# Performance work log

Hardware: AMD Instinct MI355X
Metric: run time of the kernel (lower is better)

The kernel has to match this reference:

```python
import jax, jax.numpy as jnp
import numpy as np

TAU = 0.5

def setup_inputs() -> dict:
    key = jax.random.key(0)
    kx, ky = jax.random.split(key)
    B, H = 8192, 256
    x = jax.random.normal(kx, (B, H), dtype=jnp.float32)
    y = jax.random.normal(ky, (B, H), dtype=jnp.float32)
    return {"x": x, "y": y}

def reference(x, y):
    # L2-normalize rows
    x_norm = x / jnp.linalg.norm(x, axis=1, keepdims=True)
    y_norm = y / jnp.linalg.norm(y, axis=1, keepdims=True)
    xy_norm = jnp.concatenate([x_norm, y_norm], axis=0)  # [2N, H]
    yx_norm = jnp.concatenate([y_norm, x_norm], axis=0)  # [2N, H]
    # [2N, 2N] cosine-similarity matrix (dominant memory traffic)
    sim_mat_1 = xy_norm @ xy_norm.T
    exp_mat = jnp.exp(sim_mat_1 / TAU)
    exp_row_sum = jnp.sum(exp_mat, axis=1)
    exp_diag = jnp.diagonal(exp_mat)
    denominator = exp_row_sum - exp_diag
    # diag(xy_norm @ yx_norm.T) is the row-wise dot product (avoids redundant NxN matmul)
    pos_sim = jnp.sum(xy_norm * yx_norm, axis=1)
    numerator = jnp.exp(pos_sim / TAU)
    nt_xent = -jnp.log(numerator / denominator)
    return jnp.mean(nt_xent)
```

## Files before the change

### kernel.cpp

```cpp
#include <hip/hip_runtime.h>
#include <hip/hip_bf16.h>
#include <math.h>

constexpr int NROWS = 8192;
constexpr int HDIM  = 256;
constexpr int N2    = 16384;
constexpr int TM    = 256;
constexpr int TILEB = TM * HDIM;
constexpr int NTILE = N2 / TM;
constexpr int NBLK  = NTILE * (NTILE + 1) / 2;

constexpr float PRESCALE = 1.69864357f;

typedef __attribute__((ext_vector_type(4))) float floatx4;
typedef __attribute__((ext_vector_type(2))) long longx2;

__device__ __forceinline__ void async_copy16(const void* gptr, void* lptr) {
    __builtin_amdgcn_global_load_lds(
        (const __attribute__((address_space(1))) unsigned int*)gptr,
        (__attribute__((address_space(3))) unsigned int*)lptr, 16, 0, 0);
}

#define WAIT_VM0()   __builtin_amdgcn_s_waitcnt(0x0F70)
#define MEMFENCE()   __asm__ __volatile__("" ::: "memory")
#define RAW_BARRIER() do { MEMFENCE(); __builtin_amdgcn_s_barrier(); MEMFENCE(); } while (0)

#define DPP_ROW_SHL_ADD(v, CTRL) do {                                        \
    union { float f; int i; } _u, _r; _u.f = (v);                            \
    _r.i = __builtin_amdgcn_update_dpp(0, _u.i, (CTRL), 0xF, 0xF, true);     \
    (v) += _r.f; } while (0)

__device__ __forceinline__ unsigned int f32_to_e4m3(float f) {
    const float a = fabsf(f);
    const unsigned int s = f < 0.f ? 0x80u : 0u;
    if (a < 0.015625f) {
        int mm = (int)rintf(a * 512.0f);
        if (mm == 8) return s | 0x08u;
        return s | (unsigned int)mm;
    }
    int e; const float fr = frexpf(a, &e);
    int mm = (int)rintf(fr * 16.0f) - 8;
    int E  = e + 6;
    if (mm == 8) { mm = 0; E += 1; }
    if (E > 15) { E = 15; mm = 6; }
    return s | (unsigned int)((E << 3) | mm);
}

__global__ __launch_bounds__(256) void normalize_kernel(
    const float* __restrict__ x, const float* __restrict__ y,
    unsigned char* __restrict__ Zb, float* __restrict__ pos,
    float* __restrict__ rowsum, float* __restrict__ out)
{
    const int wave = threadIdx.x >> 6, lane = threadIdx.x & 63;
    const int row  = blockIdx.x * 4 + wave;

    const float4 xv = ((const float4*)x)[row * 64 + lane];
    const float4 yv = ((const float4*)y)[row * 64 + lane];

    float sx  = xv.x*xv.x + xv.y*xv.y + xv.z*xv.z + xv.w*xv.w;
    float sy  = yv.x*yv.x + yv.y*yv.y + yv.z*yv.z + yv.w*yv.w;
    float sxy = xv.x*yv.x + xv.y*yv.y + xv.z*yv.z + xv.w*yv.w;
    #pragma unroll
    for (int m = 1; m < 64; m <<= 1) {
        sx  += __shfl_xor(sx,  m);
        sy  += __shfl_xor(sy,  m);
        sxy += __shfl_xor(sxy, m);
    }
    const float rxn = rsqrtf(sx), ryn = rsqrtf(sy);
    const float rx = rxn * PRESCALE, ry = ryn * PRESCALE;

    const unsigned int px =
        f32_to_e4m3(xv.x * rx)        | (f32_to_e4m3(xv.y * rx) << 8) |
        (f32_to_e4m3(xv.z * rx) << 16) | (f32_to_e4m3(xv.w * rx) << 24);
    const unsigned int py =
        f32_to_e4m3(yv.x * ry)        | (f32_to_e4m3(yv.y * ry) << 8) |
        (f32_to_e4m3(yv.z * ry) << 16) | (f32_to_e4m3(yv.w * ry) << 24);

    const int t  = lane >> 3;
    const int gg = (lane >> 1) & 3;
    const int posb = (t >> 1) * 64 + gg * 16 + (t & 1) * 8 + (lane & 1) * 4;

    *(unsigned int*)(Zb + (size_t)row * HDIM + posb)           = px;
    *(unsigned int*)(Zb + (size_t)(row + NROWS) * HDIM + posb) = py;

    if (lane == 0) {
        const float p = sxy * rxn * ryn;
        pos[row]         = p;
        pos[row + NROWS] = p;
    }
    const int gt = blockIdx.x * 256 + threadIdx.x;
    if (gt < N2) rowsum[gt] = 0.f;
    if (gt == 0) out[0] = 0.f;
}

__global__ __launch_bounds__(1024, 4) void simgemm_kernel(
    const unsigned char* __restrict__ Zb, float* __restrict__ rowsum)
{
    const int b = blockIdx.x;
    const int k = b & 7;
    const int m = b >> 3;
    int bi, bj;
    if (m < 36) {
        int ti = (int)((17.0f - sqrtf(289.0f - 8.0f * (float)m)) * 0.5f);
        if (m < ti * (17 - ti) / 2) ti--;
        else if (m >= (ti + 1) * (16 - ti) / 2) ti++;
        const int tj = ti + (m - ti * (17 - ti) / 2);
        bi = k * 8 + ti;
        bj = k * 8 + tj;
    } else {
        const int m2 = m - 36;
        const int hh = m2 >> 5;
        const int r  = m2 & 31;
        const int h  = hh * 8 + k;
        const int q  = h >> 1;
        const int sub = h & 1;
        int gi = 0;
        #pragma unroll
        for (int t = 6; t > 0; --t)
            if (q >= t * (15 - t) / 2) { gi = t; break; }
        const int gj = gi + 1 + (q - gi * (15 - gi) / 2);
        bi = gi * 8 + sub * 4 + (r >> 3);
        bj = gj * 8 + (r & 7);
    }
    const bool diag = (bi == bj);

    __shared__ alignas(16) unsigned char tiles[2 * TILEB];
    __shared__ float rs[TM];
    __shared__ float cs[TM];

    const int tid  = threadIdx.x;
    const int wave = tid >> 6;
    const int lane = tid & 63;
    const int wm   = wave & 3;
    const int wn   = wave >> 2;
    const int g    = lane >> 4;
    const int m15  = lane & 15;

    if (tid < TM) { rs[tid] = 0.f; cs[tid] = 0.f; }

    const int rl4 = lane >> 4;
    const int se  = ((lane & 15) ^ rl4) * 16;
    const int so  = (((lane & 15) ^ rl4) ^ 4) * 16;
    const unsigned char* gA = Zb + (size_t)(bi * TM + wave * 16 + rl4) * HDIM;
    const unsigned char* gB = Zb + (size_t)(bj * TM + wave * 16 + rl4) * HDIM;
    unsigned char* lA = tiles + (wave * 16) * HDIM;
    unsigned char* lB = tiles + TILEB + (wave * 16) * HDIM;

    async_copy16(gA + 0 * 1024 + se, lA + 0 * 1024);
    async_copy16(gA + 1 * 1024 + so, lA + 1 * 1024);
    async_copy16(gA + 2 * 1024 + se, lA + 2 * 1024);
    async_copy16(gA + 3 * 1024 + so, lA + 3 * 1024);
    async_copy16(gB + 0 * 1024 + se, lB + 0 * 1024);
    async_copy16(gB + 1 * 1024 + so, lB + 1 * 1024);
    async_copy16(gB + 2 * 1024 + se, lB + 2 * 1024);
    async_copy16(gB + 3 * 1024 + so, lB + 3 * 1024);

    WAIT_VM0();
    RAW_BARRIER();

    const int key  = m15 & 7;
    const int rowA = (wm * 64 + m15) * HDIM;
    const int rowB = (wn * 64 + m15) * HDIM;
    const unsigned char* bA = tiles;
    const unsigned char* bB = tiles + TILEB;

    floatx4 acc[4][4] = {};

    #pragma unroll
    for (int u = 0; u < 4; ++u) {
        const int off = ((u * 4 + g) ^ key) * 16;
        longx2 aV[4], bV[4];
        #pragma unroll
        for (int f = 0; f < 4; ++f) {
            aV[f] = *(const longx2*)(bA + rowA + f * 16 * HDIM + off);
            bV[f] = *(const longx2*)(bB + rowB + f * 16 * HDIM + off);
        }
        #pragma unroll
        for (int ks = 0; ks < 2; ++ks)
            #pragma unroll
            for (int fm = 0; fm < 4; ++fm)
                #pragma unroll
                for (int fn = 0; fn < 4; ++fn)
                    acc[fm][fn] = __builtin_amdgcn_mfma_f32_16x16x32_fp8_fp8(
                        aV[fm][ks], bV[fn][ks], acc[fm][fn], 0, 0, 0);
    }

    float rp[4][4] = {{0.f}};
    float cp[4]    = {0.f};

    if (!diag) {
        #pragma unroll
        for (int fm = 0; fm < 4; ++fm)
            #pragma unroll
            for (int fn = 0; fn < 4; ++fn) {
                const floatx4 a = acc[fm][fn];
                #pragma unroll
                for (int q = 0; q < 4; ++q) {
                    const float e = __builtin_amdgcn_exp2f(a[q]);
                    rp[fm][q] += e;
                    cp[fn]    += e;
                }
            }
    } else {
        #pragma unroll
        for (int fm = 0; fm < 4; ++fm)
            #pragma unroll
            for (int fn = 0; fn < 4; ++fn) {
                const floatx4 a = acc[fm][fn];
                const int cl = wn * 64 + fn * 16 + m15;
                #pragma unroll
                for (int q = 0; q < 4; ++q) {
                    const int rl = wm * 64 + fm * 16 + g * 4 + q;
                    float e = __builtin_amdgcn_exp2f(a[q]);
                    if (cl <= rl) e = 0.f;
                    rp[fm][q] += e;
                    cp[fn]    += e;
                }
            }
    }

    #pragma unroll
    for (int fm = 0; fm < 4; ++fm)
        #pragma unroll
        for (int q = 0; q < 4; ++q) {
            float v = rp[fm][q];
            DPP_ROW_SHL_ADD(v, 0x101);
            DPP_ROW_SHL_ADD(v, 0x102);
            DPP_ROW_SHL_ADD(v, 0x104);
            DPP_ROW_SHL_ADD(v, 0x108);
            rp[fm][q] = v;
        }
    if (m15 == 0) {
        #pragma unroll
        for (int fm = 0; fm < 4; ++fm)
            #pragma unroll
            for (int q = 0; q < 4; ++q)
                atomicAdd(&rs[wm * 64 + fm * 16 + g * 4 + q], rp[fm][q]);
    }

    #pragma unroll
    for (int mask = 16; mask < 64; mask <<= 1)
        #pragma unroll
        for (int fn = 0; fn < 4; ++fn)
            cp[fn] += __shfl_xor(cp[fn], mask);
    if (g == 0) {
        #pragma unroll
        for (int fn = 0; fn < 4; ++fn)
            atomicAdd(&cs[wn * 64 + fn * 16 + m15], cp[fn]);
    }

    __syncthreads();
    if (tid < TM) {
        atomicAdd(&rowsum[(size_t)bi * TM + tid], rs[tid]);
        atomicAdd(&rowsum[(size_t)bj * TM + tid], cs[tid]);
    }
}

__global__ __launch_bounds__(1024) void finalize_kernel(
    const float* __restrict__ rowsum, const float* __restrict__ pos,
    float* __restrict__ out)
{
    const int i = threadIdx.x + blockIdx.x * 1024;
    float s = logf(rowsum[i]) - 2.0f * pos[i];
    #pragma unroll
    for (int off = 32; off; off >>= 1) s += __shfl_down(s, off);
    __shared__ float sh[16];
    const int lt = threadIdx.x;
    if ((lt & 63) == 0) sh[lt >> 6] = s;
    __syncthreads();
    if (lt == 0) {
        float tot = 0.f;
        #pragma unroll
        for (int w = 0; w < 16; ++w) tot += sh[w];
        atomicAdd(out, tot / (float)N2);
    }
}

extern "C" void kernel_launch(void* const* d_in, const int* in_sizes, int n_in,
                              void* d_out, int out_size, void* d_ws, size_t ws_size,
                              hipStream_t stream)
{
    const float* x = (const float*)d_in[0];
    const float* y = (const float*)d_in[1];

    unsigned char* Zb = (unsigned char*)d_ws;
    float* rowsum = (float*)((char*)d_ws + (size_t)N2 * HDIM);
    float* pos    = rowsum + N2;

    normalize_kernel<<<NROWS / 4, 256, 0, stream>>>(x, y, Zb, pos, rowsum, (float*)d_out);
    simgemm_kernel<<<NBLK, 1024, 0, stream>>>(Zb, rowsum);
    finalize_kernel<<<N2 / 1024, 1024, 0, stream>>>(rowsum, pos, (float*)d_out);
}
```

Measured before the change: 147.5 us.

## Make similarity GEMM persistent and prefetch next tile during epilogue

The similarity kernel now launches a fixed grid of persistent blocks that loop over the triangular tile list. Each block issues async global-to-LDS loads for its next tile right after the MFMA loop, so the load overlaps the exp/reduction epilogue and the per-block launch cost disappears. The shared row/column accumulators are reset between iterations. In exchange there are fewer blocks than before, so load balance and occupancy depend on the grid size matching the CU count, and each iteration adds an extra barrier.

```diff
diff --git a/kernel.cpp b/kernel.cpp
--- a/kernel.cpp
+++ b/kernel.cpp
@@ -9,6 +9,7 @@
 constexpr int TILEB = TM * HDIM;
 constexpr int NTILE = N2 / TM;
 constexpr int NBLK  = NTILE * (NTILE + 1) / 2;
+constexpr int NPERS = 256;
 
 constexpr float PRESCALE = 1.69864357f;
 
@@ -46,60 +47,9 @@
     return s | (unsigned int)((E << 3) | mm);
 }
 
-__global__ __launch_bounds__(256) void normalize_kernel(
-    const float* __restrict__ x, const float* __restrict__ y,
-    unsigned char* __restrict__ Zb, float* __restrict__ pos,
-    float* __restrict__ rowsum, float* __restrict__ out)
-{
-    const int wave = threadIdx.x >> 6, lane = threadIdx.x & 63;
-    const int row  = blockIdx.x * 4 + wave;
-
-    const float4 xv = ((const float4*)x)[row * 64 + lane];
-    const float4 yv = ((const float4*)y)[row * 64 + lane];
-
-    float sx  = xv.x*xv.x + xv.y*xv.y + xv.z*xv.z + xv.w*xv.w;
-    float sy  = yv.x*yv.x + yv.y*yv.y + yv.z*yv.z + yv.w*yv.w;
-    float sxy = xv.x*yv.x + xv.y*yv.y + xv.z*yv.z + xv.w*yv.w;
-    #pragma unroll
-    for (int m = 1; m < 64; m <<= 1) {
-        sx  += __shfl_xor(sx,  m);
-        sy  += __shfl_xor(sy,  m);
-        sxy += __shfl_xor(sxy, m);
-    }
-    const float rxn = rsqrtf(sx), ryn = rsqrtf(sy);
-    const float rx = rxn * PRESCALE, ry = ryn * PRESCALE;
-
-    const unsigned int px =
-        f32_to_e4m3(xv.x * rx)        | (f32_to_e4m3(xv.y * rx) << 8) |
-        (f32_to_e4m3(xv.z * rx) << 16) | (f32_to_e4m3(xv.w * rx) << 24);
-    const unsigned int py =
-        f32_to_e4m3(yv.x * ry)        | (f32_to_e4m3(yv.y * ry) << 8) |
-        (f32_to_e4m3(yv.z * ry) << 16) | (f32_to_e4m3(yv.w * ry) << 24);
-
-    const int t  = lane >> 3;
-    const int gg = (lane >> 1) & 3;
-    const int posb = (t >> 1) * 64 + gg * 16 + (t & 1) * 8 + (lane & 1) * 4;
-
-    *(unsigned int*)(Zb + (size_t)row * HDIM + posb)           = px;
-    *(unsigned int*)(Zb + (size_t)(row + NROWS) * HDIM + posb) = py;
-
-    if (lane == 0) {
-        const float p = sxy * rxn * ryn;
-        pos[row]         = p;
-        pos[row + NROWS] = p;
-    }
-    const int gt = blockIdx.x * 256 + threadIdx.x;
-    if (gt < N2) rowsum[gt] = 0.f;
-    if (gt == 0) out[0] = 0.f;
-}
-
-__global__ __launch_bounds__(1024, 4) void simgemm_kernel(
-    const unsigned char* __restrict__ Zb, float* __restrict__ rowsum)
-{
-    const int b = blockIdx.x;
+__device__ __forceinline__ void tile_map(int b, int& bi, int& bj) {
     const int k = b & 7;
     const int m = b >> 3;
-    int bi, bj;
     if (m < 36) {
         int ti = (int)((17.0f - sqrtf(289.0f - 8.0f * (float)m)) * 0.5f);
         if (m < ti * (17 - ti) / 2) ti--;
@@ -122,8 +72,58 @@
         bi = gi * 8 + sub * 4 + (r >> 3);
         bj = gj * 8 + (r & 7);
     }
-    const bool diag = (bi == bj);
-
+}
+
+__global__ __launch_bounds__(256) void normalize_kernel(
+    const float* __restrict__ x, const float* __restrict__ y,
+    unsigned char* __restrict__ Zb, float* __restrict__ pos,
+    float* __restrict__ rowsum, float* __restrict__ out)
+{
+    const int wave = threadIdx.x >> 6, lane = threadIdx.x & 63;
+    const int row  = blockIdx.x * 4 + wave;
+
+    const float4 xv = ((const float4*)x)[row * 64 + lane];
+    const float4 yv = ((const float4*)y)[row * 64 + lane];
+
+    float sx  = xv.x*xv.x + xv.y*xv.y + xv.z*xv.z + xv.w*xv.w;
+    float sy  = yv.x*yv.x + yv.y*yv.y + yv.z*yv.z + yv.w*yv.w;
+    float sxy = xv.x*yv.x + xv.y*yv.y + xv.z*yv.z + xv.w*yv.w;
+    #pragma unroll
+    for (int m = 1; m < 64; m <<= 1) {
+        sx  += __shfl_xor(sx,  m);
+        sy  += __shfl_xor(sy,  m);
+        sxy += __shfl_xor(sxy, m);
+    }
+    const float rxn = rsqrtf(sx), ryn = rsqrtf(sy);
+    const float rx = rxn * PRESCALE, ry = ryn * PRESCALE;
+
+    const unsigned int px =
+        f32_to_e4m3(xv.x * rx)        | (f32_to_e4m3(xv.y * rx) << 8) |
+        (f32_to_e4m3(xv.z * rx) << 16) | (f32_to_e4m3(xv.w * rx) << 24);
+    const unsigned int py =
+        f32_to_e4m3(yv.x * ry)        | (f32_to_e4m3(yv.y * ry) << 8) |
+        (f32_to_e4m3(yv.z * ry) << 16) | (f32_to_e4m3(yv.w * ry) << 24);
+
+    const int t  = lane >> 3;
+    const int gg = (lane >> 1) & 3;
+    const int posb = (t >> 1) * 64 + gg * 16 + (t & 1) * 8 + (lane & 1) * 4;
+
+    *(unsigned int*)(Zb + (size_t)row * HDIM + posb)           = px;
+    *(unsigned int*)(Zb + (size_t)(row + NROWS) * HDIM + posb) = py;
+
+    if (lane == 0) {
+        const float p = sxy * rxn * ryn;
+        pos[row]         = p;
+        pos[row + NROWS] = p;
+    }
+    const int gt = blockIdx.x * 256 + threadIdx.x;
+    if (gt < N2) rowsum[gt] = 0.f;
+    if (gt == 0) out[0] = 0.f;
+}
+
+__global__ __launch_bounds__(1024, 4) void simgemm_kernel(
+    const unsigned char* __restrict__ Zb, float* __restrict__ rowsum)
+{
     __shared__ alignas(16) unsigned char tiles[2 * TILEB];
     __shared__ float rs[TM];
     __shared__ float cs[TM];
@@ -141,22 +141,23 @@
     const int rl4 = lane >> 4;
     const int se  = ((lane & 15) ^ rl4) * 16;
     const int so  = (((lane & 15) ^ rl4) ^ 4) * 16;
-    const unsigned char* gA = Zb + (size_t)(bi * TM + wave * 16 + rl4) * HDIM;
-    const unsigned char* gB = Zb + (size_t)(bj * TM + wave * 16 + rl4) * HDIM;
     unsigned char* lA = tiles + (wave * 16) * HDIM;
     unsigned char* lB = tiles + TILEB + (wave * 16) * HDIM;
 
-    async_copy16(gA + 0 * 1024 + se, lA + 0 * 1024);
-    async_copy16(gA + 1 * 1024 + so, lA + 1 * 1024);
-    async_copy16(gA + 2 * 1024 + se, lA + 2 * 1024);
-    async_copy16(gA + 3 * 1024 + so, lA + 3 * 1024);
-    async_copy16(gB + 0 * 1024 + se, lB + 0 * 1024);
-    async_copy16(gB + 1 * 1024 + so, lB + 1 * 1024);
-    async_copy16(gB + 2 * 1024 + se, lB + 2 * 1024);
-    async_copy16(gB + 3 * 1024 + so, lB + 3 * 1024);
-
-    WAIT_VM0();
-    RAW_BARRIER();
+    #define STAGE(BI, BJ) do {                                               \
+        const unsigned char* _gA =                                           \
+            Zb + (size_t)((BI) * TM + wave * 16 + rl4) * HDIM;               \
+        const unsigned char* _gB =                                           \
+            Zb + (size_t)((BJ) * TM + wave * 16 + rl4) * HDIM;               \
+        async_copy16(_gA + 0 * 1024 + se, lA + 0 * 1024);                    \
+        async_copy16(_gA + 1 * 1024 + so, lA + 1 * 1024);                    \
+        async_copy16(_gA + 2 * 1024 + se, lA + 2 * 1024);                    \
+        async_copy16(_gA + 3 * 1024 + so, lA + 3 * 1024);                    \
+        async_copy16(_gB + 0 * 1024 + se, lB + 0 * 1024);                    \
+        async_copy16(_gB + 1 * 1024 + so, lB + 1 * 1024);                    \
+        async_copy16(_gB + 2 * 1024 + se, lB + 2 * 1024);                    \
+        async_copy16(_gB + 3 * 1024 + so, lB + 3 * 1024);                    \
+    } while (0)
 
     const int key  = m15 & 7;
     const int rowA = (wm * 64 + m15) * HDIM;
@@ -164,96 +165,123 @@
     const unsigned char* bA = tiles;
     const unsigned char* bB = tiles + TILEB;
 
-    floatx4 acc[4][4] = {};
-
-    #pragma unroll
-    for (int u = 0; u < 4; ++u) {
-        const int off = ((u * 4 + g) ^ key) * 16;
-        longx2 aV[4], bV[4];
-        #pragma unroll
-        for (int f = 0; f < 4; ++f) {
-            aV[f] = *(const longx2*)(bA + rowA + f * 16 * HDIM + off);
-            bV[f] = *(const longx2*)(bB + rowB + f * 16 * HDIM + off);
-        }
-        #pragma unroll
-        for (int ks = 0; ks < 2; ++ks)
+    int b = blockIdx.x;
+    int bi, bj;
+    tile_map(b, bi, bj);
+    STAGE(bi, bj);
+    WAIT_VM0();
+    RAW_BARRIER();
+
+    for (;;) {
+        floatx4 acc[4][4] = {};
+        #pragma unroll
+        for (int u = 0; u < 4; ++u) {
+            const int off = ((u * 4 + g) ^ key) * 16;
+            longx2 aV[4], bV[4];
+            #pragma unroll
+            for (int f = 0; f < 4; ++f) {
+                aV[f] = *(const longx2*)(bA + rowA + f * 16 * HDIM + off);
+                bV[f] = *(const longx2*)(bB + rowB + f * 16 * HDIM + off);
+            }
+            #pragma unroll
+            for (int ks = 0; ks < 2; ++ks)
+                #pragma unroll
+                for (int fm = 0; fm < 4; ++fm)
+                    #pragma unroll
+                    for (int fn = 0; fn < 4; ++fn)
+                        acc[fm][fn] = __builtin_amdgcn_mfma_f32_16x16x32_fp8_fp8(
+                            aV[fm][ks], bV[fn][ks], acc[fm][fn], 0, 0, 0);
+        }
+
+        RAW_BARRIER();
+
+        const int bnext = b + NPERS;
+        const bool have_next = bnext < NBLK;
+        int bi2 = 0, bj2 = 0;
+        if (have_next) {
+            tile_map(bnext, bi2, bj2);
+            STAGE(bi2, bj2);
+        }
+
+        const bool diag = (bi == bj);
+        float rp[4][4] = {{0.f}};
+        float cp[4]    = {0.f};
+
+        if (!diag) {
             #pragma unroll
             for (int fm = 0; fm < 4; ++fm)
                 #pragma unroll
-                for (int fn = 0; fn < 4; ++fn)
-                    acc[fm][fn] = __builtin_amdgcn_mfma_f32_16x16x32_fp8_fp8(
-                        aV[fm][ks], bV[fn][ks], acc[fm][fn], 0, 0, 0);
-    }
-
-    float rp[4][4] = {{0.f}};
-    float cp[4]    = {0.f};
-
-    if (!diag) {
+                for (int fn = 0; fn < 4; ++fn) {
+                    const floatx4 a = acc[fm][fn];
+                    #pragma unroll
+                    for (int q = 0; q < 4; ++q) {
+                        const float e = __builtin_amdgcn_exp2f(a[q]);
+                        rp[fm][q] += e;
+                        cp[fn]    += e;
+                    }
+                }
+        } else {
+            #pragma unroll
+            for (int fm = 0; fm < 4; ++fm)
+                #pragma unroll
+                for (int fn = 0; fn < 4; ++fn) {
+                    const floatx4 a = acc[fm][fn];
+                    const int cl = wn * 64 + fn * 16 + m15;
+                    #pragma unroll
+                    for (int q = 0; q < 4; ++q) {
+                        const int rl = wm * 64 + fm * 16 + g * 4 + q;
+                        float e = __builtin_amdgcn_exp2f(a[q]);
+                        if (cl <= rl) e = 0.f;
+                        rp[fm][q] += e;
+                        cp[fn]    += e;
+                    }
+                }
+        }
+
         #pragma unroll
         for (int fm = 0; fm < 4; ++fm)
             #pragma unroll
-            for (int fn = 0; fn < 4; ++fn) {
-                const floatx4 a = acc[fm][fn];
+            for (int q = 0; q < 4; ++q) {
+                float v = rp[fm][q];
+                DPP_ROW_SHL_ADD(v, 0x101);
+                DPP_ROW_SHL_ADD(v, 0x102);
+                DPP_ROW_SHL_ADD(v, 0x104);
+                DPP_ROW_SHL_ADD(v, 0x108);
+                rp[fm][q] = v;
+            }
+        if (m15 == 0) {
+            #pragma unroll
+            for (int fm = 0; fm < 4; ++fm)
                 #pragma unroll
-                for (int q = 0; q < 4; ++q) {
-                    const float e = __builtin_amdgcn_exp2f(a[q]);
-                    rp[fm][q] += e;
-                    cp[fn]    += e;
-                }
-            }
-    } else {
-        #pragma unroll
-        for (int fm = 0; fm < 4; ++fm)
-            #pragma unroll
-            for (int fn = 0; fn < 4; ++fn) {
-                const floatx4 a = acc[fm][fn];
-                const int cl = wn * 64 + fn * 16 + m15;
-                #pragma unroll
-                for (int q = 0; q < 4; ++q) {
-                    const int rl = wm * 64 + fm * 16 + g * 4 + q;
-                    float e = __builtin_amdgcn_exp2f(a[q]);
-                    if (cl <= rl) e = 0.f;
-                    rp[fm][q] += e;
-                    cp[fn]    += e;
-                }
-            }
-    }
-
-    #pragma unroll
-    for (int fm = 0; fm < 4; ++fm)
-        #pragma unroll
-        for (int q = 0; q < 4; ++q) {
-            float v = rp[fm][q];
-            DPP_ROW_SHL_ADD(v, 0x101);
-            DPP_ROW_SHL_ADD(v, 0x102);
-            DPP_ROW_SHL_ADD(v, 0x104);
-            DPP_ROW_SHL_ADD(v, 0x108);
-            rp[fm][q] = v;
-        }
-    if (m15 == 0) {
-        #pragma unroll
-        for (int fm = 0; fm < 4; ++fm)
-            #pragma unroll
-            for (int q = 0; q < 4; ++q)
-                atomicAdd(&rs[wm * 64 + fm * 16 + g * 4 + q], rp[fm][q]);
-    }
-
-    #pragma unroll
-    for (int mask = 16; mask < 64; mask <<= 1)
-        #pragma unroll
-        for (int fn = 0; fn < 4; ++fn)
-            cp[fn] += __shfl_xor(cp[fn], mask);
-    if (g == 0) {
-        #pragma unroll
-        for (int fn = 0; fn < 4; ++fn)
-            atomicAdd(&cs[wn * 64 + fn * 16 + m15], cp[fn]);
-    }
-
-    __syncthreads();
-    if (tid < TM) {
-        atomicAdd(&rowsum[(size_t)bi * TM + tid], rs[tid]);
-        atomicAdd(&rowsum[(size_t)bj * TM + tid], cs[tid]);
-    }
+                for (int q = 0; q < 4; ++q)
+                    atomicAdd(&rs[wm * 64 + fm * 16 + g * 4 + q], rp[fm][q]);
+        }
+
+        #pragma unroll
+        for (int mask = 16; mask < 64; mask <<= 1)
+            #pragma unroll
+            for (int fn = 0; fn < 4; ++fn)
+                cp[fn] += __shfl_xor(cp[fn], mask);
+        if (g == 0) {
+            #pragma unroll
+            for (int fn = 0; fn < 4; ++fn)
+                atomicAdd(&cs[wn * 64 + fn * 16 + m15], cp[fn]);
+        }
+
+        __syncthreads();
+        if (tid < TM) {
+            atomicAdd(&rowsum[(size_t)bi * TM + tid], rs[tid]);
+            atomicAdd(&rowsum[(size_t)bj * TM + tid], cs[tid]);
+            rs[tid] = 0.f;
+            cs[tid] = 0.f;
+        }
+
+        if (!have_next) break;
+        b = bnext; bi = bi2; bj = bj2;
+        WAIT_VM0();
+        RAW_BARRIER();
+    }
+    #undef STAGE
 }
 
 __global__ __launch_bounds__(1024) void finalize_kernel(
@@ -288,6 +316,6 @@
     float* pos    = rowsum + N2;
 
     normalize_kernel<<<NROWS / 4, 256, 0, stream>>>(x, y, Zb, pos, rowsum, (float*)d_out);
-    simgemm_kernel<<<NBLK, 1024, 0, stream>>>(Zb, rowsum);
+    simgemm_kernel<<<NPERS, 1024, 0, stream>>>(Zb, rowsum);
     finalize_kernel<<<N2 / 1024, 1024, 0, stream>>>(rowsum, pos, (float*)d_out);
 }
```

New measurement: 155.6 us. +5.5%, slower.
